# Kernel optimization log

Measured on AMD Instinct MI355X. Metric: run time of the kernel, lower is better.

The kernel has to match this reference:

```python
import jax, jax.numpy as jnp
import numpy as np

B, S, D, H = 2, 2048, 1024, 16
DH = D // H
EPS = 1e-5


def setup_inputs() -> dict:
    key = jax.random.key(0)
    ks = jax.random.split(key, 12)
    inp = {
        "Q_source": jax.random.normal(ks[0], (B, S, D), jnp.float32),
        "K_source": jax.random.normal(ks[1], (B, S, D), jnp.float32),
        "V_source": jax.random.normal(ks[2], (B, S, D), jnp.float32),
        "padding_mask": jnp.zeros((B, 1, 1, S), dtype=bool),  # no padded keys (avoids NaN rows)
        "future_mask": jnp.triu(jnp.ones((S, S), dtype=bool), k=1)[None, None],  # causal
    }
    sc = 1.0 / np.sqrt(D)
    names = ["WQ", "WK", "WV", "WO"]
    for i, n in enumerate(names):
        inp[n] = jax.random.normal(ks[3 + i], (D, D), jnp.float32) * sc
        inp["b" + n[1]] = jnp.zeros((D,), jnp.float32)
    inp["gamma"] = jnp.ones((D,), jnp.float32)
    inp["beta"] = jnp.zeros((D,), jnp.float32)
    return inp


def reference(Q_source, K_source, V_source, padding_mask, future_mask,
              WQ, bQ, WK, bK, WV, bV, WO, bO, gamma, beta):
    b = Q_source.shape[0]
    # torch Linear: x @ W.T + b ; reshape to [B, H, S, DH]
    def proj(x, W, bb):
        y = x @ W.T + bb
        return y.reshape(b, -1, H, DH).transpose(0, 2, 1, 3)

    Q = proj(Q_source, WQ, bQ)
    K = proj(K_source, WK, bK)
    V = proj(V_source, WV, bV)

    scores = jnp.einsum("bhqd,bhkd->bhqk", Q, K) / jnp.sqrt(jnp.float32(DH))
    neg_inf = jnp.float32(-jnp.inf)
    scores = jnp.where(padding_mask, neg_inf, scores)
    scores = jnp.where(future_mask, neg_inf, scores)
    attn = jax.nn.softmax(scores, axis=-1)

    ctx = jnp.einsum("bhqk,bhkd->bhqd", attn, V)
    ctx = ctx.transpose(0, 2, 1, 3).reshape(b, -1, D)
    out = ctx @ WO.T + bO

    x = Q_source + out
    mu = x.mean(-1, keepdims=True)
    var = x.var(-1, keepdims=True)
    return (x - mu) * jax.lax.rsqrt(var + EPS) * gamma + beta
```

## Files before the change

### kernel.cpp

```cpp
#include <hip/hip_runtime.h>

#define S_LEN 2048
#define DMODEL 1024
#define NH 16
#define DHD 64

typedef __attribute__((ext_vector_type(8))) short bh8;
typedef __attribute__((ext_vector_type(4))) float f32x4;
typedef __attribute__((ext_vector_type(2))) unsigned int u32x2;
typedef __attribute__((ext_vector_type(4))) unsigned int u32x4;
typedef unsigned short u16;
typedef unsigned int u32;

static __device__ __forceinline__ u16 f2bf(float f) {
    unsigned u = __builtin_bit_cast(unsigned, f);
    u += 0x7fffu + ((u >> 16) & 1u);
    return (u16)(u >> 16);
}

typedef const __attribute__((address_space(1))) void* gptr_t;
typedef __attribute__((address_space(3))) void* lptr_t;

static __device__ __forceinline__ void gll16(const void* g, void* l) {
    __builtin_amdgcn_global_load_lds((gptr_t)g, (lptr_t)l, 16, 0, 0);
}

__global__ __launch_bounds__(256) void cvt_all(const float* __restrict__ WQ, const float* __restrict__ WK,
                                               const float* __restrict__ WV, const float* __restrict__ WO,
                                               const float* __restrict__ S0, const float* __restrict__ S1,
                                               const float* __restrict__ S2,
                                               u16* __restrict__ wq, u16* __restrict__ wk,
                                               u16* __restrict__ wv, u16* __restrict__ wo,
                                               u16* __restrict__ q0, u16* __restrict__ k0,
                                               u16* __restrict__ v0) {
    int bid = blockIdx.x;
    const float* s;
    u16* o;
    size_t base;
    if (bid < 2048) {
        int wi = bid >> 9;
        s = wi == 0 ? WQ : (wi == 1 ? WK : (wi == 2 ? WV : WO));
        o = wi == 0 ? wq : (wi == 1 ? wk : (wi == 2 ? wv : wo));
        base = (size_t)(bid & 511) * 2048;
    } else {
        int r = bid - 2048;
        int si = r >> 11;
        s = si == 0 ? S0 : (si == 1 ? S1 : S2);
        o = si == 0 ? q0 : (si == 1 ? k0 : v0);
        base = (size_t)(r & 2047) * 2048;
    }
    size_t i = base + (size_t)threadIdx.x * 8;
    float4 a = *(const float4*)(s + i);
    float4 b = *(const float4*)(s + i + 4);
    u32 p0 = (u32)f2bf(a.x) | ((u32)f2bf(a.y) << 16);
    u32 p1 = (u32)f2bf(a.z) | ((u32)f2bf(a.w) << 16);
    u32 p2 = (u32)f2bf(b.x) | ((u32)f2bf(b.y) << 16);
    u32 p3 = (u32)f2bf(b.z) | ((u32)f2bf(b.w) << 16);
    *(u32x4*)(o + i) = (u32x4){p0, p1, p2, p3};
}

template <int BM, int OBF, int AF32>
static __device__ __forceinline__ void gemm_body(const void* __restrict__ Ap, const u16* __restrict__ Bm,
                                                 const float* __restrict__ bias, void* __restrict__ Cv,
                                                 int N, int K, int bi, int bj, short* Al, short* Bl,
                                                 float oscale) {
    constexpr int MI = BM / 32;
    constexpr int NC = BM / 64;
    int tid = threadIdx.x, lane = tid & 63, w = tid >> 6;
    int ln = lane & 15, hi = lane >> 4;
    int wm = w >> 1, wn = w & 1;
    f32x4 acc[MI][4];
#pragma unroll
    for (int i = 0; i < MI; i++)
#pragma unroll
        for (int j = 0; j < 4; j++) acc[i][j] = (f32x4){0.f, 0.f, 0.f, 0.f};
    int nk = K >> 5;

    float4 fa[NC][2];
    auto loadA = [&](int kt) {
#pragma unroll
        for (int c = 0; c < NC; ++c) {
            int o = c * 4096 + tid * 16;
            int row = o >> 6, e0 = (o & 63) >> 1;
            const float* src = (const float*)Ap + (size_t)(bi * BM + row) * K + kt * 32 + e0;
            fa[c][0] = *(const float4*)src;
            fa[c][1] = *(const float4*)(src + 4);
        }
    };
    auto writeA = [&](int buf) {
#pragma unroll
        for (int c = 0; c < NC; ++c) {
            int o = c * 4096 + tid * 16;
            u32 w0 = (u32)f2bf(fa[c][0].x) | ((u32)f2bf(fa[c][0].y) << 16);
            u32 w1 = (u32)f2bf(fa[c][0].z) | ((u32)f2bf(fa[c][0].w) << 16);
            u32 w2 = (u32)f2bf(fa[c][1].x) | ((u32)f2bf(fa[c][1].y) << 16);
            u32 w3 = (u32)f2bf(fa[c][1].z) | ((u32)f2bf(fa[c][1].w) << 16);
            *(u32x4*)((char*)(Al + buf * (BM * 32)) + o) = (u32x4){w0, w1, w2, w3};
        }
    };
    auto stageA_lds = [&](int buf, int kt) {
#pragma unroll
        for (int c = 0; c < NC; ++c) {
            int o = c * 4096 + tid * 16;
            int row = o >> 6, col = (o & 63) >> 1;
            gll16((const u16*)Ap + (size_t)(bi * BM + row) * K + kt * 32 + col,
                  (char*)(Al + buf * (BM * 32)) + o);
        }
    };
    auto stageB = [&](int buf, int kt) {
#pragma unroll
        for (int c = 0; c < 2; ++c) {
            int o = c * 4096 + tid * 16;
            int row = o >> 6, col = (o & 63) >> 1;
            gll16(Bm + (size_t)(bj * 128 + row) * K + kt * 32 + col, (char*)(Bl + buf * 4096) + o);
        }
    };

    if constexpr (AF32) { loadA(0); writeA(0); } else { stageA_lds(0, 0); }
    stageB(0, 0);
    __syncthreads();
    int cur = 0;
    for (int kt = 0; kt < nk; ++kt) {
        bool pre = (kt + 1 < nk);
        if (pre) {
            if constexpr (AF32) loadA(kt + 1); else stageA_lds(cur ^ 1, kt + 1);
            stageB(cur ^ 1, kt + 1);
        }
        bh8 av[MI], bv[4];
#pragma unroll
        for (int i = 0; i < MI; i++) av[i] = *(const bh8*)&Al[cur * (BM * 32) + (wm * (BM / 2) + i * 16 + ln) * 32 + hi * 8];
#pragma unroll
        for (int j = 0; j < 4; j++) bv[j] = *(const bh8*)&Bl[cur * 4096 + (wn * 64 + j * 16 + ln) * 32 + hi * 8];
#pragma unroll
        for (int i = 0; i < MI; i++)
#pragma unroll
            for (int j = 0; j < 4; j++)
                acc[i][j] = __builtin_amdgcn_mfma_f32_16x16x32_bf16(av[i], bv[j], acc[i][j], 0, 0, 0);
        if constexpr (AF32) { if (pre) writeA(cur ^ 1); }
        __syncthreads();
        cur ^= 1;
    }
    if constexpr (OBF == 2) {
#pragma unroll
        for (int j = 0; j < 4; j++) {
            int col = wn * 64 + j * 16 + ln;
            float bvs = bias[bj * 128 + col];
#pragma unroll
            for (int i = 0; i < MI; i++) {
                int row0 = wm * (BM / 2) + i * 16 + hi * 4;
                u32 p01 = (u32)f2bf(acc[i][j][0] + bvs) | ((u32)f2bf(acc[i][j][1] + bvs) << 16);
                u32 p23 = (u32)f2bf(acc[i][j][2] + bvs) | ((u32)f2bf(acc[i][j][3] + bvs) << 16);
                int idx = col * 128 + (row0 ^ ((col & 7) << 3));
                *(u32x2*)&Al[idx] = (u32x2){p01, p23};
            }
        }
        __syncthreads();
        int b = bi >> 4;
        int sbase = (bi & 15) * 128;
#pragma unroll
        for (int it = 0; it < 8; ++it) {
            int idx = it * 256 + tid;
            int dcol = idx >> 4;
            int sl = (idx & 15) * 8;
            bh8 v = *(const bh8*)&Al[dcol * 128 + (sl ^ ((dcol & 7) << 3))];
            int h = bj * 2 + (dcol >> 6), d = dcol & 63;
            *(bh8*)((u16*)Cv + ((size_t)((b * 16 + h) * 64 + d)) * 2048 + sbase + sl) = v;
        }
        return;
    }
#pragma unroll
    for (int j = 0; j < 4; j++) {
        int col = bj * 128 + wn * 64 + j * 16 + ln;
        float bvs = bias[col];
#pragma unroll
        for (int i = 0; i < MI; i++) {
            int row0 = bi * BM + wm * (BM / 2) + i * 16 + hi * 4;
#pragma unroll
            for (int rr = 0; rr < 4; rr++) {
                if (OBF) {
                    float v = (acc[i][j][rr] + bvs) * oscale;
                    ((u16*)Cv)[(size_t)(row0 + rr) * N + col] = f2bf(v);
                } else {
                    ((float*)Cv)[(size_t)(row0 + rr) * N + col] = acc[i][j][rr] + bvs;
                }
            }
        }
    }
}

__global__ __launch_bounds__(256, 3) void gemm_qkv(const u16* __restrict__ A0, const u16* __restrict__ A1,
                                                   const u16* __restrict__ A2, const u16* __restrict__ B0,
                                                   const u16* __restrict__ B1, const u16* __restrict__ B2,
                                                   const float* __restrict__ c0, const float* __restrict__ c1,
                                                   const float* __restrict__ c2, u16* __restrict__ C0,
                                                   u16* __restrict__ C1, u16* __restrict__ VT) {
    __shared__ short SH[16384];
    short* Al = SH;
    short* Bl = SH + 8192;
    int bid = blockIdx.x;
    int swz = (bid & 7) * 96 + (bid >> 3);
    int z = swz >> 8, t = swz & 255;
    if (z == 2) {
        gemm_body<128, 2, 0>(A2, B2, c2, VT, 1024, 1024, t >> 3, t & 7, Al, Bl, 1.0f);
    } else if (z == 0) {
        gemm_body<128, 1, 0>(A0, B0, c0, C0, 1024, 1024, t >> 3, t & 7, Al, Bl, 0.18033688f);
    } else {
        gemm_body<128, 1, 0>(A1, B1, c1, C1, 1024, 1024, t >> 3, t & 7, Al, Bl, 1.0f);
    }
}

__global__ __launch_bounds__(512, 4) void gemm_o(const u16* __restrict__ A, const u16* __restrict__ Bm,
                                                 const float* __restrict__ bias, const float* __restrict__ Res,
                                                 float* __restrict__ C) {
    __shared__ short Al[2 * 64 * 32];
    __shared__ short Bl[2 * 128 * 32];
    int tid = threadIdx.x, lane = tid & 63, w = tid >> 6;
    int ln = lane & 15, hi = lane >> 4;
    int wm = w >> 2, wn = w & 3;
    int bid = blockIdx.x;
    int swz = (bid & 7) * 64 + (bid >> 3);
    int bi = swz >> 3, bj = swz & 7;
    f32x4 acc[2][2];
#pragma unroll
    for (int i = 0; i < 2; i++)
#pragma unroll
        for (int j = 0; j < 2; j++) acc[i][j] = (f32x4){0.f, 0.f, 0.f, 0.f};

    auto stageA = [&](int buf, int kt) {
        if (tid < 256) {
            int o = tid * 16;
            int row = o >> 6, col = (o & 63) >> 1;
            gll16(A + (size_t)(bi * 64 + row) * 1024 + kt * 32 + col, (char*)(Al + buf * 2048) + o);
        }
    };
    auto stageB = [&](int buf, int kt) {
        int o = tid * 16;
        int row = o >> 6, col = (o & 63) >> 1;
        gll16(Bm + (size_t)(bj * 128 + row) * 1024 + kt * 32 + col, (char*)(Bl + buf * 4096) + o);
    };

    stageA(0, 0);
    stageB(0, 0);
    __syncthreads();
    int cur = 0;
    for (int kt = 0; kt < 32; ++kt) {
        if (kt + 1 < 32) {
            stageA(cur ^ 1, kt + 1);
            stageB(cur ^ 1, kt + 1);
        }
        bh8 av[2], bv[2];
#pragma unroll
        for (int i = 0; i < 2; i++) av[i] = *(const bh8*)&Al[cur * 2048 + (wm * 32 + i * 16 + ln) * 32 + hi * 8];
#pragma unroll
        for (int j = 0; j < 2; j++) bv[j] = *(const bh8*)&Bl[cur * 4096 + (wn * 32 + j * 16 + ln) * 32 + hi * 8];
#pragma unroll
        for (int i = 0; i < 2; i++)
#pragma unroll
            for (int j = 0; j < 2; j++)
                acc[i][j] = __builtin_amdgcn_mfma_f32_16x16x32_bf16(av[i], bv[j], acc[i][j], 0, 0, 0);
        __syncthreads();
        cur ^= 1;
    }
#pragma unroll
    for (int j = 0; j < 2; j++) {
        int col = bj * 128 + wn * 32 + j * 16 + ln;
        float bvs = bias[col];
#pragma unroll
        for (int i = 0; i < 2; i++) {
            int row0 = bi * 64 + wm * 32 + i * 16 + hi * 4;
#pragma unroll
            for (int rr = 0; rr < 4; rr++) {
                size_t idx = (size_t)(row0 + rr) * 1024 + col;
                C[idx] = acc[i][j][rr] + bvs + Res[idx];
            }
        }
    }
}

template <int PLO, int PHI>
static __device__ __forceinline__ void attn_core(const u16* __restrict__ Qp, const u16* __restrict__ Kp,
                                                 const u16* __restrict__ VT, u16* __restrict__ Ctx,
                                                 short* Klb, short* Vlb, short* Pw, float* Csh, float* Ls,
                                                 int b, int h, int bh, int qt, int tid) {
    int lane = tid & 63, w = tid >> 6;
    int grp = w >> 2;
    int qsub = w & 3;
    int tgl = tid & 255;
    int ln = lane & 15, hi = lane >> 4;
    __builtin_amdgcn_s_setprio(PLO);
    bh8 ones;
#pragma unroll
    for (int e = 0; e < 8; e++) ones[e] = (short)0x3F80;

    auto stage_kv = [&](int buf, int kt) {
#pragma unroll
        for (int c = 0; c < 2; ++c) {
            int o = c * 4096 + tgl * 16;
            int rr = o >> 7;
            int slot = (o >> 4) & 7;
            gll16(Kp + ((size_t)(b * S_LEN + kt * 64 + rr)) * DMODEL + h * DHD + ((slot ^ (rr & 7)) << 3),
                  (char*)(Klb + buf * 4096) + o);
            gll16(VT + ((size_t)(bh * DHD + rr)) * S_LEN + kt * 64 + ((slot ^ (rr & 7)) << 3),
                  (char*)(Vlb + buf * 4096) + o);
        }
    };

    int nh = qt + 1;
    int nt = 2 * qt + 2;
    int kbase = grp * nh;
    int qg0 = (qt << 7) + qsub * 32 + ln;
    const bh8* qr0 = (const bh8*)(Qp + ((size_t)(b * S_LEN + qg0)) * DMODEL + h * DHD);
    const bh8* qr1 = (const bh8*)(Qp + ((size_t)(b * S_LEN + qg0 + 16)) * DMODEL + h * DHD);
    bh8 qf[2][2];
    qf[0][0] = qr0[hi]; qf[0][1] = qr0[4 + hi];
    qf[1][0] = qr1[hi]; qf[1][1] = qr1[4 + hi];
    f32x4 ctxa[2][4];
    f32x4 lacc[2];
#pragma unroll
    for (int g = 0; g < 2; g++) {
        lacc[g] = (f32x4){0.f, 0.f, 0.f, 0.f};
#pragma unroll
        for (int i = 0; i < 4; i++) ctxa[g][i] = (f32x4){0.f, 0.f, 0.f, 0.f};
    }
    stage_kv(0, kbase);
    if (nh > 1) stage_kv(1, kbase + 1);
    __syncthreads();
    for (int i = 0; i < nh; i += 2) {
        int s = i >> 1;
        int b0 = (s & 1) << 1;
        int b1 = b0 + 1;
        bool two = (i + 1 < nh);
        if (i + 2 < nh) stage_kv(b0 ^ 2, kbase + i + 2);
        if (i + 3 < nh) stage_kv(b1 ^ 2, kbase + i + 3);
        int kt0 = kbase + i;
        int kt1 = kbase + i + 1;
        f32x4 scA[2][4], scB[2][4];
#pragma unroll
        for (int g = 0; g < 2; g++)
#pragma unroll
            for (int ks = 0; ks < 4; ++ks) { scA[g][ks] = (f32x4){0.f, 0.f, 0.f, 0.f}; scB[g][ks] = (f32x4){0.f, 0.f, 0.f, 0.f}; }
        __builtin_amdgcn_s_setprio(PHI);
#pragma unroll
        for (int dwin = 0; dwin < 2; ++dwin) {
#pragma unroll
            for (int ks = 0; ks < 4; ++ks) {
                int rr = ks * 16 + ln;
                bh8 kv = *(const bh8*)&Klb[b0 * 4096 + rr * 64 + ((dwin * 32 + hi * 8) ^ ((rr & 7) << 3))];
                scA[0][ks] = __builtin_amdgcn_mfma_f32_16x16x32_bf16(kv, qf[0][dwin], scA[0][ks], 0, 0, 0);
                scA[1][ks] = __builtin_amdgcn_mfma_f32_16x16x32_bf16(kv, qf[1][dwin], scA[1][ks], 0, 0, 0);
            }
        }
        if (two) {
#pragma unroll
            for (int dwin = 0; dwin < 2; ++dwin) {
#pragma unroll
                for (int ks = 0; ks < 4; ++ks) {
                    int rr = ks * 16 + ln;
                    bh8 kv = *(const bh8*)&Klb[b1 * 4096 + rr * 64 + ((dwin * 32 + hi * 8) ^ ((rr & 7) << 3))];
                    scB[0][ks] = __builtin_amdgcn_mfma_f32_16x16x32_bf16(kv, qf[0][dwin], scB[0][ks], 0, 0, 0);
                    scB[1][ks] = __builtin_amdgcn_mfma_f32_16x16x32_bf16(kv, qf[1][dwin], scB[1][ks], 0, 0, 0);
                }
            }
        }
        __builtin_amdgcn_s_setprio(PLO);
        if (kt0 >= nt - 2) {
#pragma unroll
            for (int g = 0; g < 2; g++) {
                int qgq = qg0 + g * 16;
#pragma unroll
                for (int ks = 0; ks < 4; ++ks)
#pragma unroll
                    for (int rr = 0; rr < 4; ++rr) {
                        int kg = kt0 * 64 + ks * 16 + hi * 4 + rr;
                        scA[g][ks][rr] = (kg <= qgq) ? scA[g][ks][rr] : -1e30f;
                    }
            }
        }
#pragma unroll
        for (int g = 0; g < 2; g++) {
#pragma unroll
            for (int ks = 0; ks < 4; ++ks) {
                u32 u0 = __builtin_bit_cast(u32, __builtin_amdgcn_exp2f(scA[g][ks][0]));
                u32 u1 = __builtin_bit_cast(u32, __builtin_amdgcn_exp2f(scA[g][ks][1]));
                u32 u2 = __builtin_bit_cast(u32, __builtin_amdgcn_exp2f(scA[g][ks][2]));
                u32 u3 = __builtin_bit_cast(u32, __builtin_amdgcn_exp2f(scA[g][ks][3]));
                u32 a01 = (u0 >> 16) | (u1 & 0xffff0000u);
                u32 a23 = (u2 >> 16) | (u3 & 0xffff0000u);
                int kloc = ks * 16 + hi * 4;
                *(u32x2*)&Pw[(g * 16 + ln) * 64 + (kloc ^ ((ln & 7) << 3))] = (u32x2){a01, a23};
            }
        }
        __builtin_amdgcn_s_setprio(PHI);
#pragma unroll
        for (int kw = 0; kw < 2; ++kw) {
            bh8 pf0 = *(const bh8*)&Pw[ln * 64 + ((kw * 32 + hi * 8) ^ ((ln & 7) << 3))];
            bh8 pf1 = *(const bh8*)&Pw[(16 + ln) * 64 + ((kw * 32 + hi * 8) ^ ((ln & 7) << 3))];
            lacc[0] = __builtin_amdgcn_mfma_f32_16x16x32_bf16(ones, pf0, lacc[0], 0, 0, 0);
            lacc[1] = __builtin_amdgcn_mfma_f32_16x16x32_bf16(ones, pf1, lacc[1], 0, 0, 0);
#pragma unroll
            for (int ds = 0; ds < 4; ++ds) {
                int d = ds * 16 + ln;
                bh8 vf = *(const bh8*)&Vlb[b0 * 4096 + d * 64 + ((kw * 32 + hi * 8) ^ ((d & 7) << 3))];
                ctxa[0][ds] = __builtin_amdgcn_mfma_f32_16x16x32_bf16(vf, pf0, ctxa[0][ds], 0, 0, 0);
                ctxa[1][ds] = __builtin_amdgcn_mfma_f32_16x16x32_bf16(vf, pf1, ctxa[1][ds], 0, 0, 0);
            }
        }
        __builtin_amdgcn_s_setprio(PLO);
        if (two) {
            if (kt1 >= nt - 2) {
#pragma unroll
                for (int g = 0; g < 2; g++) {
                    int qgq = qg0 + g * 16;
#pragma unroll
                    for (int ks = 0; ks < 4; ++ks)
#pragma unroll
                        for (int rr = 0; rr < 4; ++rr) {
                            int kg = kt1 * 64 + ks * 16 + hi * 4 + rr;
                            scB[g][ks][rr] = (kg <= qgq) ? scB[g][ks][rr] : -1e30f;
                        }
                }
            }
#pragma unroll
            for (int g = 0; g < 2; g++) {
#pragma unroll
                for (int ks = 0; ks < 4; ++ks) {
                    u32 u0 = __builtin_bit_cast(u32, __builtin_amdgcn_exp2f(scB[g][ks][0]));
                    u32 u1 = __builtin_bit_cast(u32, __builtin_amdgcn_exp2f(scB[g][ks][1]));
                    u32 u2 = __builtin_bit_cast(u32, __builtin_amdgcn_exp2f(scB[g][ks][2]));
                    u32 u3 = __builtin_bit_cast(u32, __builtin_amdgcn_exp2f(scB[g][ks][3]));
                    u32 a01 = (u0 >> 16) | (u1 & 0xffff0000u);
                    u32 a23 = (u2 >> 16) | (u3 & 0xffff0000u);
                    int kloc = ks * 16 + hi * 4;
                    *(u32x2*)&Pw[(g * 16 + ln) * 64 + (kloc ^ ((ln & 7) << 3))] = (u32x2){a01, a23};
                }
            }
            __builtin_amdgcn_s_setprio(PHI);
#pragma unroll
            for (int kw = 0; kw < 2; ++kw) {
                bh8 pf0 = *(const bh8*)&Pw[ln * 64 + ((kw * 32 + hi * 8) ^ ((ln & 7) << 3))];
                bh8 pf1 = *(const bh8*)&Pw[(16 + ln) * 64 + ((kw * 32 + hi * 8) ^ ((ln & 7) << 3))];
                lacc[0] = __builtin_amdgcn_mfma_f32_16x16x32_bf16(ones, pf0, lacc[0], 0, 0, 0);
                lacc[1] = __builtin_amdgcn_mfma_f32_16x16x32_bf16(ones, pf1, lacc[1], 0, 0, 0);
#pragma unroll
                for (int ds = 0; ds < 4; ++ds) {
                    int d = ds * 16 + ln;
                    bh8 vf = *(const bh8*)&Vlb[b1 * 4096 + d * 64 + ((kw * 32 + hi * 8) ^ ((d & 7) << 3))];
                    ctxa[0][ds] = __builtin_amdgcn_mfma_f32_16x16x32_bf16(vf, pf0, ctxa[0][ds], 0, 0, 0);
                    ctxa[1][ds] = __builtin_amdgcn_mfma_f32_16x16x32_bf16(vf, pf1, ctxa[1][ds], 0, 0, 0);
                }
            }
            __builtin_amdgcn_s_setprio(PLO);
        }
        __syncthreads();
    }
    __builtin_amdgcn_s_setprio(0);
    if (grp == 1) {
#pragma unroll
        for (int g = 0; g < 2; g++) {
            int qloc = g * 16 + ln;
#pragma unroll
            for (int ds = 0; ds < 4; ++ds) {
                int doff = (ds * 16 + hi * 4) ^ ((qloc & 7) << 3);
                *(f32x4*)&Csh[(qsub * 32 + qloc) * 64 + doff] = ctxa[g][ds];
            }
            if (hi == 0) Ls[qsub * 32 + qloc] = lacc[g][0];
        }
    }
    __syncthreads();
    if (grp == 0) {
#pragma unroll
        for (int g = 0; g < 2; g++) {
            int qloc = g * 16 + ln;
            float inv = 1.f / (lacc[g][0] + Ls[qsub * 32 + qloc]);
            u16* cp = Ctx + ((size_t)(b * S_LEN + qg0 + g * 16)) * DMODEL + h * DHD;
#pragma unroll
            for (int ds = 0; ds < 4; ++ds) {
                int doff = (ds * 16 + hi * 4) ^ ((qloc & 7) << 3);
                f32x4 p = *(const f32x4*)&Csh[(qsub * 32 + qloc) * 64 + doff];
                ushort4 st;
                st.x = f2bf((ctxa[g][ds][0] + p[0]) * inv);
                st.y = f2bf((ctxa[g][ds][1] + p[1]) * inv);
                st.z = f2bf((ctxa[g][ds][2] + p[2]) * inv);
                st.w = f2bf((ctxa[g][ds][3] + p[3]) * inv);
                *(ushort4*)(cp + ds * 16 + hi * 4) = st;
            }
        }
    }
}

__global__ __launch_bounds__(512, 1) void attn_fwd(const u16* __restrict__ Qp, const u16* __restrict__ Kp,
                                                   const u16* __restrict__ VT, u16* __restrict__ Ctx) {
    __shared__ short Kl[2][4][4096];
    __shared__ short Vl[2][4][4096];
    __shared__ short Pl[8][2048];
    int tid = threadIdx.x, w = tid >> 6;
    int grp = w >> 2;
    int bid = blockIdx.x;
    int rnd = bid >> 8, slot = bid & 255;
    int xcd = slot & 7, t = slot >> 3;
    int bh = xcd * 4 + (t & 3);
    int qte = t >> 2;
    int qt = rnd ? (15 - 2 * qte) : (2 * qte);
    int b = bh >> 4, h = bh & 15;
    float* Csh = (float*)&Kl[0][0][0];
    float* Ls = (float*)&Pl[7][1024];
    if (qt >= 8)
        attn_core<2, 3>(Qp, Kp, VT, Ctx, &Kl[grp][0][0], &Vl[grp][0][0], &Pl[w][0], Csh, Ls, b, h, bh, qt, tid);
    else
        attn_core<0, 1>(Qp, Kp, VT, Ctx, &Kl[grp][0][0], &Vl[grp][0][0], &Pl[w][0], Csh, Ls, b, h, bh, qt, tid);
}

__global__ __launch_bounds__(256) void ln_res(const float* __restrict__ Y,
                                              const float* __restrict__ gamma, const float* __restrict__ beta,
                                              float* __restrict__ out) {
    int row = blockIdx.x, tid = threadIdx.x;
    const float4* yr = (const float4*)(Y + (size_t)row * DMODEL);
    float4 a = yr[tid];
    float x0 = a.x, x1 = a.y, x2 = a.z, x3 = a.w;
    float s1 = x0 + x1 + x2 + x3;
    float s2 = x0 * x0 + x1 * x1 + x2 * x2 + x3 * x3;
#pragma unroll
    for (int off = 32; off > 0; off >>= 1) {
        s1 += __shfl_xor(s1, off);
        s2 += __shfl_xor(s2, off);
    }
    __shared__ float r1[4], r2[4];
    int wv = tid >> 6;
    if ((tid & 63) == 0) { r1[wv] = s1; r2[wv] = s2; }
    __syncthreads();
    s1 = r1[0] + r1[1] + r1[2] + r1[3];
    s2 = r2[0] + r2[1] + r2[2] + r2[3];
    float mu = s1 * (1.0f / 1024.0f);
    float var = s2 * (1.0f / 1024.0f) - mu * mu;
    float rstd = rsqrtf(var + 1e-5f);
    const float4* g4 = (const float4*)gamma;
    const float4* b4 = (const float4*)beta;
    float4 g = g4[tid], bb = b4[tid];
    float4 res;
    res.x = (x0 - mu) * rstd * g.x + bb.x;
    res.y = (x1 - mu) * rstd * g.y + bb.y;
    res.z = (x2 - mu) * rstd * g.z + bb.z;
    res.w = (x3 - mu) * rstd * g.w + bb.w;
    *((float4*)(out + (size_t)row * DMODEL) + tid) = res;
}

extern "C" void kernel_launch(void* const* d_in, const int* in_sizes, int n_in,
                              void* d_out, int out_size, void* d_ws, size_t ws_size,
                              hipStream_t stream) {
    const float* Qs = (const float*)d_in[0];
    const float* Ks = (const float*)d_in[1];
    const float* Vs = (const float*)d_in[2];
    const float* WQ = (const float*)d_in[5];
    const float* bQ = (const float*)d_in[6];
    const float* WK = (const float*)d_in[7];
    const float* bK = (const float*)d_in[8];
    const float* WV = (const float*)d_in[9];
    const float* bV = (const float*)d_in[10];
    const float* WO = (const float*)d_in[11];
    const float* bO = (const float*)d_in[12];
    const float* gamma = (const float*)d_in[13];
    const float* beta = (const float*)d_in[14];

    const size_t MB = 1u << 20;
    char* w8 = (char*)d_ws;
    u16* Qb  = (u16*)(w8 + 0 * MB);
    u16* Kb  = (u16*)(w8 + 8 * MB);
    u16* Vb  = (u16*)(w8 + 16 * MB);
    u16* WQb = (u16*)(w8 + 24 * MB);
    u16* WKb = (u16*)(w8 + 26 * MB);
    u16* WVb = (u16*)(w8 + 28 * MB);
    u16* WOb = (u16*)(w8 + 30 * MB);
    u16* Qp  = (u16*)(w8 + 32 * MB);
    u16* Kp  = (u16*)(w8 + 40 * MB);
    u16* VTb = (u16*)(w8 + 56 * MB);
    u16* Ctx = (u16*)(w8 + 64 * MB);
    float* Y2 = (float*)(w8 + 72 * MB);

    cvt_all<<<8192, 256, 0, stream>>>(WQ, WK, WV, WO, Qs, Ks, Vs, WQb, WKb, WVb, WOb, Qb, Kb, Vb);
    gemm_qkv<<<768, 256, 0, stream>>>(Qb, Kb, Vb, WQb, WKb, WVb, bQ, bK, bV, Qp, Kp, VTb);
    attn_fwd<<<512, 512, 0, stream>>>(Qp, Kp, VTb, Ctx);
    gemm_o<<<512, 512, 0, stream>>>(Ctx, WOb, bO, Qs, Y2);
    ln_res<<<4096, 256, 0, stream>>>(Y2, gamma, beta, (float*)d_out);
}
```

Measured before the change: 109.8 us.

## Split K across warp groups in output projection GEMM with LDS reduction

The output-projection GEMM now splits the K dimension in half between two groups of four warps. Each warp computes a 32x64 sub-tile over 512 of K, and the partial sums from the second group are reduced through a swizzled LDS buffer before the epilogue. This halves the serial K-loop iterations and barriers and gives each warp more MFMAs per LDS load. In exchange it uses more shared memory (48KB), more accumulator registers, and an extra LDS reduction pass, which may lower occupancy.

```diff
diff --git a/kernel.cpp b/kernel.cpp
--- a/kernel.cpp
+++ b/kernel.cpp
@@ -212,66 +212,88 @@
 __global__ __launch_bounds__(512, 4) void gemm_o(const u16* __restrict__ A, const u16* __restrict__ Bm,
                                                  const float* __restrict__ bias, const float* __restrict__ Res,
                                                  float* __restrict__ C) {
-    __shared__ short Al[2 * 64 * 32];
-    __shared__ short Bl[2 * 128 * 32];
+    __shared__ char SH[49152];
     int tid = threadIdx.x, lane = tid & 63, w = tid >> 6;
     int ln = lane & 15, hi = lane >> 4;
-    int wm = w >> 2, wn = w & 3;
+    int kh = w >> 2;
+    int wq = w & 3;
+    int wm = wq >> 1, wn = wq & 1;
+    int tgl = tid & 255;
     int bid = blockIdx.x;
     int swz = (bid & 7) * 64 + (bid >> 3);
     int bi = swz >> 3, bj = swz & 7;
-    f32x4 acc[2][2];
+    f32x4 acc[2][4];
 #pragma unroll
     for (int i = 0; i < 2; i++)
 #pragma unroll
-        for (int j = 0; j < 2; j++) acc[i][j] = (f32x4){0.f, 0.f, 0.f, 0.f};
-
+        for (int j = 0; j < 4; j++) acc[i][j] = (f32x4){0.f, 0.f, 0.f, 0.f};
+
+    auto Alp = [&](int buf) { return (short*)(SH + kh * 8192 + buf * 4096); };
+    auto Blp = [&](int buf) { return (short*)(SH + 16384 + kh * 16384 + buf * 8192); };
     auto stageA = [&](int buf, int kt) {
-        if (tid < 256) {
-            int o = tid * 16;
-            int row = o >> 6, col = (o & 63) >> 1;
-            gll16(A + (size_t)(bi * 64 + row) * 1024 + kt * 32 + col, (char*)(Al + buf * 2048) + o);
-        }
+        int o = tgl * 16;
+        int row = o >> 6, col = (o & 63) >> 1;
+        gll16(A + (size_t)(bi * 64 + row) * 1024 + kh * 512 + kt * 32 + col, (char*)Alp(buf) + o);
     };
     auto stageB = [&](int buf, int kt) {
-        int o = tid * 16;
-        int row = o >> 6, col = (o & 63) >> 1;
-        gll16(Bm + (size_t)(bj * 128 + row) * 1024 + kt * 32 + col, (char*)(Bl + buf * 4096) + o);
+#pragma unroll
+        for (int c = 0; c < 2; ++c) {
+            int o = c * 4096 + tgl * 16;
+            int row = o >> 6, col = (o & 63) >> 1;
+            gll16(Bm + (size_t)(bj * 128 + row) * 1024 + kh * 512 + kt * 32 + col, (char*)Blp(buf) + o);
+        }
     };
 
     stageA(0, 0);
     stageB(0, 0);
     __syncthreads();
     int cur = 0;
-    for (int kt = 0; kt < 32; ++kt) {
-        if (kt + 1 < 32) {
+    for (int kt = 0; kt < 16; ++kt) {
+        if (kt + 1 < 16) {
             stageA(cur ^ 1, kt + 1);
             stageB(cur ^ 1, kt + 1);
         }
-        bh8 av[2], bv[2];
-#pragma unroll
-        for (int i = 0; i < 2; i++) av[i] = *(const bh8*)&Al[cur * 2048 + (wm * 32 + i * 16 + ln) * 32 + hi * 8];
-#pragma unroll
-        for (int j = 0; j < 2; j++) bv[j] = *(const bh8*)&Bl[cur * 4096 + (wn * 32 + j * 16 + ln) * 32 + hi * 8];
+        bh8 av[2], bv[4];
+#pragma unroll
+        for (int i = 0; i < 2; i++) av[i] = *(const bh8*)&Alp(cur)[(wm * 32 + i * 16 + ln) * 32 + hi * 8];
+#pragma unroll
+        for (int j = 0; j < 4; j++) bv[j] = *(const bh8*)&Blp(cur)[(wn * 64 + j * 16 + ln) * 32 + hi * 8];
 #pragma unroll
         for (int i = 0; i < 2; i++)
 #pragma unroll
-            for (int j = 0; j < 2; j++)
+            for (int j = 0; j < 4; j++)
                 acc[i][j] = __builtin_amdgcn_mfma_f32_16x16x32_bf16(av[i], bv[j], acc[i][j], 0, 0, 0);
         __syncthreads();
         cur ^= 1;
     }
-#pragma unroll
-    for (int j = 0; j < 2; j++) {
-        int col = bj * 128 + wn * 32 + j * 16 + ln;
-        float bvs = bias[col];
-#pragma unroll
-        for (int i = 0; i < 2; i++) {
-            int row0 = bi * 64 + wm * 32 + i * 16 + hi * 4;
-#pragma unroll
-            for (int rr = 0; rr < 4; rr++) {
-                size_t idx = (size_t)(row0 + rr) * 1024 + col;
-                C[idx] = acc[i][j][rr] + bvs + Res[idx];
+    float* Csh = (float*)SH;
+    if (kh == 1) {
+#pragma unroll
+        for (int j = 0; j < 4; j++) {
+            int col = wn * 64 + j * 16 + ln;
+#pragma unroll
+            for (int i = 0; i < 2; i++) {
+                int r0 = wm * 32 + i * 16 + hi * 4;
+                *(f32x4*)&Csh[col * 64 + (r0 ^ ((col & 7) << 2))] = acc[i][j];
+            }
+        }
+    }
+    __syncthreads();
+    if (kh == 0) {
+#pragma unroll
+        for (int j = 0; j < 4; j++) {
+            int col = wn * 64 + j * 16 + ln;
+            int colg = bj * 128 + col;
+            float bvs = bias[colg];
+#pragma unroll
+            for (int i = 0; i < 2; i++) {
+                int r0 = wm * 32 + i * 16 + hi * 4;
+                f32x4 p = *(const f32x4*)&Csh[col * 64 + (r0 ^ ((col & 7) << 2))];
+#pragma unroll
+                for (int rr = 0; rr < 4; rr++) {
+                    size_t idx = (size_t)(bi * 64 + r0 + rr) * 1024 + colg;
+                    C[idx] = acc[i][j][rr] + p[rr] + bvs + Res[idx];
+                }
             }
         }
     }
```

Result: faster. 107.2 us (-2.4%).
